# Kernel tuning notes

Hardware: AMD Instinct MI355X
Metric: run time of the kernel (lower is better)

The kernel has to match this reference:

```python
import jax, jax.numpy as jnp
import numpy as np

B, T, N, D = 64, 12, 512, 2      # batch, seq_len, num_nodes, input_dim
R, M, O, H = 64, 64, 1, 12       # rnn_units, message_size, output_dim, horizon


def setup_inputs() -> dict:
    key = jax.random.key(0)
    ks = jax.random.split(key, 12)
    inputs = jax.random.normal(ks[0], (B, T, N, D), jnp.float32)
    h0 = jax.random.normal(ks[1], (N, B, R), jnp.float32)  # torch.randn initial state
    adj = jax.random.uniform(ks[2], (N, N), jnp.float32)
    mask = jax.random.uniform(ks[3], (N, N)) < 0.05
    adj = jnp.where(mask, adj, 0.0)
    s = 1.0 / np.sqrt(R)
    u = lambda k, shape: jax.random.uniform(k, shape, jnp.float32, -s, s)
    return {
        "inputs": inputs, "h0": h0, "adj": adj,
        "W_msg": u(ks[4], (M, R)), "b_msg": u(ks[5], (M,)),
        "W_ih": u(ks[6], (3 * R, D + M)), "W_hh": u(ks[7], (3 * R, R)),
        "b_ih": u(ks[8], (3 * R,)), "b_hh": u(ks[9], (3 * R,)),
        "W_out": u(ks[10], (O * H, R)), "b_out": u(ks[11], (O * H,)),
    }


def reference(inputs, h0, adj, W_msg, b_msg, W_ih, W_hh, b_ih, b_hh, W_out, b_out):
    # mask matches the 'adj[j,i] > 0' guard in the python double loop
    adj_pos = jnp.where(adj > 0.0, adj, 0.0)

    def step(h, x_t):
        # h: [N, B, R]; x_t: [B, N, D]
        hw = h @ W_msg.T + b_msg                       # M_t(h): [N, B, M]
        # m[i] = sum_j adj[j, i] * hw[j]  -> dense masked aggregation
        m = jnp.einsum('ji,jbm->ibm', adj_pos, hw)     # [N, B, M]
        inp2 = jnp.concatenate([m, jnp.transpose(x_t, (1, 0, 2))], axis=2)  # [N, B, M+D]
        # torch GRUCell math (elementwise over the N*B 'batch'):
        gi = inp2 @ W_ih.T + b_ih                      # [N, B, 3R]
        gh = h @ W_hh.T + b_hh                         # [N, B, 3R]
        i_r, i_z, i_n = jnp.split(gi, 3, axis=-1)
        h_r, h_z, h_n = jnp.split(gh, 3, axis=-1)
        r = jax.nn.sigmoid(i_r + h_r)
        z = jax.nn.sigmoid(i_z + h_z)
        n = jnp.tanh(i_n + r * h_n)
        h_new = (1.0 - z) * n + z * h
        return h_new, None

    xs = jnp.transpose(inputs, (1, 0, 2, 3))           # [T, B, N, D]
    h, _ = jax.lax.scan(step, h0, xs)                  # [N, B, R]
    out = h @ W_out.T + b_out                          # R_t(h): [N, B, O*H]
    out = out.reshape(N, B, H, O)                      # reshape(N, B, horizon, -1)
    return jnp.transpose(out, (1, 2, 0, 3))            # [B, H, N, O]
```

## Files before the change

### kernel.cpp

```cpp
#include <hip/hip_runtime.h>

#define Bb 64
#define Tt 12
#define Nn 512
#define Dd 2
#define G3 192
#define Hh 12

typedef float f32x4 __attribute__((ext_vector_type(4)));
typedef _Float16 f16;
typedef _Float16 f16x8 __attribute__((ext_vector_type(8)));

__device__ __forceinline__ int swz4(int row, int bo) {
  return row * 256 + (bo ^ ((row & 7) << 4));
}

__global__ __launch_bounds__(256) void init_kernel(
    const float* __restrict__ adj, const float* __restrict__ W_msg,
    const float* __restrict__ W_ih, const float* __restrict__ W_hh,
    const float* __restrict__ b_ih, const float* __restrict__ b_hh,
    const float* __restrict__ b_msg, f16* __restrict__ g_atf,
    float* __restrict__ g_rowsum, f16* __restrict__ g_w,
    float* __restrict__ g_f) {
  const int bid = blockIdx.x, tid = threadIdx.x, l = tid & 63, wt = tid >> 6;
  if (bid < 32) {
    const int it = bid;
    for (int kt = wt; kt < 16; kt += 4) {
      const int i = (it << 4) + (l & 15);
      const int j0 = (kt << 5) + ((l >> 4) << 3);
      f16* dhi = g_atf + ((it * 16 + kt) * 2 + 0) * 512 + l * 8;
      f16* dlo = g_atf + ((it * 16 + kt) * 2 + 1) * 512 + l * 8;
#pragma unroll
      for (int e = 0; e < 8; ++e) {
        float a = adj[(j0 + e) * Nn + i];
        a = a > 0.f ? a : 0.f;
        const f16 h = (f16)a;
        dhi[e] = h;
        dlo[e] = (f16)(a - (float)h);
      }
    }
    {
      const int i = (it << 4) + (tid >> 4);
      float rs = 0.f;
      for (int j = (tid & 15); j < Nn; j += 16) {
        const float a = adj[j * Nn + i];
        rs += (a > 0.f ? a : 0.f);
      }
      for (int off = 8; off; off >>= 1) rs += __shfl_down(rs, off, 16);
      if ((tid & 15) == 0) g_rowsum[i] = rs;
    }
  } else if (bid == 40) {
    for (int tile = wt; tile < 24; tile += 4) {
      const int nt = tile >> 1, kt = tile & 1;
      const int wrow = nt * 16 + (l & 15);
      const int kc = kt * 32 + ((l >> 4) << 3);
      const float* s2 = W_ih + wrow * 66 + kc;
      const float* s1 = W_hh + wrow * 64 + kc;
#pragma unroll
      for (int j = 0; j < 8; ++j) {
        g_w[tile * 512 + l * 8 + j] = (f16)s2[j];
        g_w[12288 + tile * 512 + l * 8 + j] = (f16)s1[j];
      }
    }
    for (int tile = wt; tile < 8; tile += 4) {
      const int nt = tile >> 1, kt = tile & 1;
      const int wrow = nt * 16 + (l & 15);
      const int kc = kt * 32 + ((l >> 4) << 3);
      const float* s1 = W_msg + wrow * 64 + kc;
#pragma unroll
      for (int j = 0; j < 8; ++j) g_w[24576 + tile * 512 + l * 8 + j] = (f16)s1[j];
    }
    if (tid < G3) {
      g_f[tid * 2] = W_ih[tid * 66 + 64];
      g_f[tid * 2 + 1] = W_ih[tid * 66 + 65];
      g_f[384 + tid] = b_ih[tid];
      g_f[576 + tid] = b_hh[tid];
    }
    if (tid < 64) g_f[768 + tid] = b_msg[tid];
  }
}

__global__ __launch_bounds__(256, 2) void agg_kernel(
    const float* __restrict__ h_src, const f16* __restrict__ g_atf,
    float* __restrict__ s_out) {
  const int bx = blockIdx.x, tid = threadIdx.x, l = tid & 63, wt = tid >> 6;
  const int bi = bx >> 6, bc = bx & 63;
  const int c0 = bc << 6;
  const int it = (bi << 2) + wt;

  const int cl = l & 15;
  const int jk = (l >> 4) << 3;
  const float* hp = h_src + (size_t)jk * 4096 + c0 + cl;
  const f16* ap = g_atf + (it * 16) * 2 * 512 + l * 8;

  f32x4 acc[4];
#pragma unroll
  for (int nt = 0; nt < 4; ++nt) acc[nt] = (f32x4){0.f, 0.f, 0.f, 0.f};

#pragma unroll 4
  for (int kt = 0; kt < 16; ++kt) {
    float v[32];
#pragma unroll
    for (int nt = 0; nt < 4; ++nt)
#pragma unroll
      for (int e = 0; e < 8; ++e)
        v[nt * 8 + e] = hp[(size_t)(kt * 32 + e) * 4096 + nt * 16];

    const f16x8 ahi = *(const f16x8*)(ap + (kt * 2 + 0) * 512);
    const f16x8 alo = *(const f16x8*)(ap + (kt * 2 + 1) * 512);
#pragma unroll
    for (int nt = 0; nt < 4; ++nt) {
      f16x8 bhi, blo;
#pragma unroll
      for (int e = 0; e < 8; ++e) {
        const float x = v[nt * 8 + e];
        const f16 h = (f16)x;
        bhi[e] = h;
        blo[e] = (f16)(x - (float)h);
      }
      acc[nt] = __builtin_amdgcn_mfma_f32_16x16x32_f16(ahi, bhi, acc[nt], 0, 0, 0);
      acc[nt] = __builtin_amdgcn_mfma_f32_16x16x32_f16(alo, bhi, acc[nt], 0, 0, 0);
      acc[nt] = __builtin_amdgcn_mfma_f32_16x16x32_f16(ahi, blo, acc[nt], 0, 0, 0);
    }
  }

  const int ib = (it << 4) + ((l >> 4) << 2);
#pragma unroll
  for (int nt = 0; nt < 4; ++nt) {
    const int col = c0 + (nt << 4) + cl;
#pragma unroll
    for (int g = 0; g < 4; ++g)
      s_out[(ib + g) * 4096 + col] = acc[nt][g];
  }
}

__global__ __launch_bounds__(256, 2) void step_kernel(
    const float* __restrict__ xin, const float* __restrict__ h_src,
    float* __restrict__ h_ws, const float* __restrict__ s_in,
    const uint4* __restrict__ g_blob, const float* __restrict__ g_rowsum,
    const float* __restrict__ W_out, const float* __restrict__ b_out,
    float* __restrict__ out, int t) {
  __shared__ uint4 sBlob[3840];
  __shared__ float m_lds[4096];
  const f16* sBih = (const f16*)sBlob;
  const f16* sBhh = sBih + 12288;
  const f16* sBmsg = sBih + 24576;
  const float* sF = (const float*)(sBih + 28672);
  const float* sWx = sF;
  const float* s_bih = sF + 384;
  const float* s_bhh = sF + 576;
  const float* s_bmsg = sF + 768;

  const int n = blockIdx.x, tid = threadIdx.x, l = tid & 63, wt = tid >> 6;
  const int ar = wt * 16 + (l & 15);
  const int kc = (l >> 4) << 3;

  float x0[4], x1[4];
#pragma unroll
  for (int g = 0; g < 4; ++g) {
    const int brow = wt * 16 + ((l >> 4) << 2) + g;
    const float2 xv = *(const float2*)(xin + ((brow * Tt + t) * Nn + n) * Dd);
    x0[g] = xv.x;
    x1[g] = xv.y;
  }
  const float rsum = g_rowsum[n];
  const float* hrow = h_src + n * 4096;
  const float* srow = s_in + n * 4096;

  f16x8 shi0, slo0, shi1, slo1;
  {
    const float4 q0 = *(const float4*)(srow + ar * 64 + kc);
    const float4 q1 = *(const float4*)(srow + ar * 64 + kc + 4);
    const float4 q2 = *(const float4*)(srow + ar * 64 + 32 + kc);
    const float4 q3 = *(const float4*)(srow + ar * 64 + 36 + kc);
    const float v[16] = {q0.x, q0.y, q0.z, q0.w, q1.x, q1.y, q1.z, q1.w,
                         q2.x, q2.y, q2.z, q2.w, q3.x, q3.y, q3.z, q3.w};
#pragma unroll
    for (int j = 0; j < 8; ++j) {
      f16 h = (f16)v[j];       shi0[j] = h; slo0[j] = (f16)(v[j] - (float)h);
      f16 g = (f16)v[8 + j];   shi1[j] = g; slo1[j] = (f16)(v[8 + j] - (float)g);
    }
  }
  f16x8 ahi0, alo0, ahi1, alo1;
  {
    const float4 q0 = *(const float4*)(hrow + ar * 64 + kc);
    const float4 q1 = *(const float4*)(hrow + ar * 64 + kc + 4);
    const float4 q2 = *(const float4*)(hrow + ar * 64 + 32 + kc);
    const float4 q3 = *(const float4*)(hrow + ar * 64 + 36 + kc);
    const float v[16] = {q0.x, q0.y, q0.z, q0.w, q1.x, q1.y, q1.z, q1.w,
                         q2.x, q2.y, q2.z, q2.w, q3.x, q3.y, q3.z, q3.w};
#pragma unroll
    for (int j = 0; j < 8; ++j) {
      f16 h = (f16)v[j];       ahi0[j] = h; alo0[j] = (f16)(v[j] - (float)h);
      f16 g = (f16)v[8 + j];   ahi1[j] = g; alo1[j] = (f16)(v[8 + j] - (float)g);
    }
  }
  float hreg[4][4];
#pragma unroll
  for (int ct = 0; ct < 4; ++ct)
#pragma unroll
    for (int g = 0; g < 4; ++g) {
      const int row = wt * 16 + ((l >> 4) << 2) + g;
      hreg[ct][g] = hrow[row * 64 + ct * 16 + (l & 15)];
    }
  for (int i = tid; i < 3840; i += 256) sBlob[i] = g_blob[i];
  __syncthreads();

  {
    f32x4 cm[4];
#pragma unroll
    for (int nt = 0; nt < 4; ++nt) {
      cm[nt] = (f32x4){0.f, 0.f, 0.f, 0.f};
      const f16x8 b0 = *(const f16x8*)(sBmsg + (nt * 2 + 0) * 512 + l * 8);
      const f16x8 b1 = *(const f16x8*)(sBmsg + (nt * 2 + 1) * 512 + l * 8);
      cm[nt] = __builtin_amdgcn_mfma_f32_16x16x32_f16(shi0, b0, cm[nt], 0, 0, 0);
      cm[nt] = __builtin_amdgcn_mfma_f32_16x16x32_f16(slo0, b0, cm[nt], 0, 0, 0);
      cm[nt] = __builtin_amdgcn_mfma_f32_16x16x32_f16(shi1, b1, cm[nt], 0, 0, 0);
      cm[nt] = __builtin_amdgcn_mfma_f32_16x16x32_f16(slo1, b1, cm[nt], 0, 0, 0);
    }
#pragma unroll
    for (int nt = 0; nt < 4; ++nt) {
      const int col = nt * 16 + (l & 15);
      const float bm = rsum * s_bmsg[col];
#pragma unroll
      for (int g = 0; g < 4; ++g) {
        const int row = wt * 16 + ((l >> 4) << 2) + g;
        *(float*)((char*)m_lds + swz4(row, col * 4)) = cm[nt][g] + bm;
      }
    }
  }
  f16x8 mhi0, mlo0, mhi1, mlo1;
  {
    const float4 p0 = *(const float4*)((const char*)m_lds + swz4(ar, kc * 4));
    const float4 p1 = *(const float4*)((const char*)m_lds + swz4(ar, kc * 4 + 16));
    const float4 p2 = *(const float4*)((const char*)m_lds + swz4(ar, 128 + kc * 4));
    const float4 p3 = *(const float4*)((const char*)m_lds + swz4(ar, 128 + kc * 4 + 16));
    const float v[16] = {p0.x, p0.y, p0.z, p0.w, p1.x, p1.y, p1.z, p1.w,
                         p2.x, p2.y, p2.z, p2.w, p3.x, p3.y, p3.z, p3.w};
#pragma unroll
    for (int j = 0; j < 8; ++j) {
      f16 h = (f16)v[j];       mhi0[j] = h; mlo0[j] = (f16)(v[j] - (float)h);
      f16 g = (f16)v[8 + j];   mhi1[j] = g; mlo1[j] = (f16)(v[8 + j] - (float)g);
    }
  }

  f32x4 cgi[12], cgh[12];
#pragma unroll
  for (int nt = 0; nt < 12; ++nt) {
    cgi[nt] = (f32x4){0.f, 0.f, 0.f, 0.f};
    cgh[nt] = (f32x4){0.f, 0.f, 0.f, 0.f};
  }
#pragma unroll
  for (int nt = 0; nt < 12; ++nt) {
    const f16x8 bh0 = *(const f16x8*)(sBhh + (nt * 2 + 0) * 512 + l * 8);
    const f16x8 bh1 = *(const f16x8*)(sBhh + (nt * 2 + 1) * 512 + l * 8);
    cgh[nt] = __builtin_amdgcn_mfma_f32_16x16x32_f16(ahi0, bh0, cgh[nt], 0, 0, 0);
    cgh[nt] = __builtin_amdgcn_mfma_f32_16x16x32_f16(alo0, bh0, cgh[nt], 0, 0, 0);
    cgh[nt] = __builtin_amdgcn_mfma_f32_16x16x32_f16(ahi1, bh1, cgh[nt], 0, 0, 0);
    cgh[nt] = __builtin_amdgcn_mfma_f32_16x16x32_f16(alo1, bh1, cgh[nt], 0, 0, 0);
    const f16x8 bi0 = *(const f16x8*)(sBih + (nt * 2 + 0) * 512 + l * 8);
    const f16x8 bi1 = *(const f16x8*)(sBih + (nt * 2 + 1) * 512 + l * 8);
    cgi[nt] = __builtin_amdgcn_mfma_f32_16x16x32_f16(mhi0, bi0, cgi[nt], 0, 0, 0);
    cgi[nt] = __builtin_amdgcn_mfma_f32_16x16x32_f16(mlo0, bi0, cgi[nt], 0, 0, 0);
    cgi[nt] = __builtin_amdgcn_mfma_f32_16x16x32_f16(mhi1, bi1, cgi[nt], 0, 0, 0);
    cgi[nt] = __builtin_amdgcn_mfma_f32_16x16x32_f16(mlo1, bi1, cgi[nt], 0, 0, 0);
  }

#pragma unroll
  for (int ct = 0; ct < 4; ++ct) {
    const int colr = ct * 16 + (l & 15);
    const float wr0 = sWx[colr * 2], wr1 = sWx[colr * 2 + 1];
    const float wz0 = sWx[(colr + 64) * 2], wz1 = sWx[(colr + 64) * 2 + 1];
    const float wn0 = sWx[(colr + 128) * 2], wn1 = sWx[(colr + 128) * 2 + 1];
    const float bir = s_bih[colr], biz = s_bih[colr + 64], bin_ = s_bih[colr + 128];
    const float bhr = s_bhh[colr], bhz = s_bhh[colr + 64], bhn = s_bhh[colr + 128];
#pragma unroll
    for (int g = 0; g < 4; ++g) {
      const int row = wt * 16 + ((l >> 4) << 2) + g;
      const float gir = cgi[ct][g] + x0[g] * wr0 + x1[g] * wr1 + bir;
      const float giz = cgi[ct + 4][g] + x0[g] * wz0 + x1[g] * wz1 + biz;
      const float gin = cgi[ct + 8][g] + x0[g] * wn0 + x1[g] * wn1 + bin_;
      const float ghr = cgh[ct][g] + bhr;
      const float ghz = cgh[ct + 4][g] + bhz;
      const float ghn = cgh[ct + 8][g] + bhn;
      const float rg = 1.f / (1.f + __expf(-(gir + ghr)));
      const float zg = 1.f / (1.f + __expf(-(giz + ghz)));
      const float pa = gin + rg * ghn;
      const float e2 = __expf(-2.f * fabsf(pa));
      float th = (1.f - e2) / (1.f + e2);
      th = copysignf(th, pa);
      const float hn = (1.f - zg) * th + zg * hreg[ct][g];
      if (t < Tt - 1) {
        h_ws[n * 4096 + row * 64 + colr] = hn;
      } else {
        *(float*)((char*)m_lds + swz4(row, colr * 4)) = hn;
      }
    }
  }

  if (t == Tt - 1) {
    f16x8 ohi0, olo0, ohi1, olo1;
    {
      const float4 p0 = *(const float4*)((const char*)m_lds + swz4(ar, kc * 4));
      const float4 p1 = *(const float4*)((const char*)m_lds + swz4(ar, kc * 4 + 16));
      const float4 p2 = *(const float4*)((const char*)m_lds + swz4(ar, 128 + kc * 4));
      const float4 p3 = *(const float4*)((const char*)m_lds + swz4(ar, 128 + kc * 4 + 16));
      const float v[16] = {p0.x, p0.y, p0.z, p0.w, p1.x, p1.y, p1.z, p1.w,
                           p2.x, p2.y, p2.z, p2.w, p3.x, p3.y, p3.z, p3.w};
#pragma unroll
      for (int j = 0; j < 8; ++j) {
        f16 h = (f16)v[j];       ohi0[j] = h; olo0[j] = (f16)(v[j] - (float)h);
        f16 g = (f16)v[8 + j];   ohi1[j] = g; olo1[j] = (f16)(v[8 + j] - (float)g);
      }
    }
    const int o = l & 15;
    f16x8 wo0 = {0, 0, 0, 0, 0, 0, 0, 0}, wo1 = {0, 0, 0, 0, 0, 0, 0, 0};
    if (o < Hh) {
      const float* wr_ = W_out + o * 64 + kc;
      const float4 w0 = *(const float4*)(wr_);
      const float4 w1 = *(const float4*)(wr_ + 4);
      const float4 w2 = *(const float4*)(wr_ + 32);
      const float4 w3 = *(const float4*)(wr_ + 36);
      wo0[0] = (f16)w0.x; wo0[1] = (f16)w0.y; wo0[2] = (f16)w0.z; wo0[3] = (f16)w0.w;
      wo0[4] = (f16)w1.x; wo0[5] = (f16)w1.y; wo0[6] = (f16)w1.z; wo0[7] = (f16)w1.w;
      wo1[0] = (f16)w2.x; wo1[1] = (f16)w2.y; wo1[2] = (f16)w2.z; wo1[3] = (f16)w2.w;
      wo1[4] = (f16)w3.x; wo1[5] = (f16)w3.y; wo1[6] = (f16)w3.z; wo1[7] = (f16)w3.w;
    }
    f32x4 c = {0.f, 0.f, 0.f, 0.f};
    c = __builtin_amdgcn_mfma_f32_16x16x32_f16(ohi0, wo0, c, 0, 0, 0);
    c = __builtin_amdgcn_mfma_f32_16x16x32_f16(olo0, wo0, c, 0, 0, 0);
    c = __builtin_amdgcn_mfma_f32_16x16x32_f16(ohi1, wo1, c, 0, 0, 0);
    c = __builtin_amdgcn_mfma_f32_16x16x32_f16(olo1, wo1, c, 0, 0, 0);
    if (o < Hh) {
      const float bo_ = b_out[o];
#pragma unroll
      for (int g = 0; g < 4; ++g) {
        const int b = wt * 16 + ((l >> 4) << 2) + g;
        out[(b * Hh + o) * Nn + n] = c[g] + bo_;
      }
    }
  }
}

extern "C" void kernel_launch(void* const* d_in, const int* in_sizes, int n_in,
                              void* d_out, int out_size, void* d_ws, size_t ws_size,
                              hipStream_t stream) {
  const float* xin = (const float*)d_in[0];
  const float* h0 = (const float*)d_in[1];
  const float* adj = (const float*)d_in[2];
  const float* W_msg = (const float*)d_in[3];
  const float* b_msg = (const float*)d_in[4];
  const float* W_ih = (const float*)d_in[5];
  const float* W_hh = (const float*)d_in[6];
  const float* b_ih = (const float*)d_in[7];
  const float* b_hh = (const float*)d_in[8];
  const float* W_out = (const float*)d_in[9];
  const float* b_out = (const float*)d_in[10];
  float* out = (float*)d_out;

  char* ws = (char*)d_ws;
  float* h_ws = (float*)ws;
  float* s_buf = (float*)(ws + (8u << 20));
  f16* g_atf = (f16*)(ws + (16u << 20));
  char* base = ws + (17u << 20);
  f16* g_w = (f16*)base;
  float* g_f = (float*)(base + 57344);
  float* g_rowsum = (float*)(base + 61440);
  const uint4* g_blob = (const uint4*)base;

  init_kernel<<<48, 256, 0, stream>>>(adj, W_msg, W_ih, W_hh, b_ih, b_hh,
                                      b_msg, g_atf, g_rowsum, g_w, g_f);
  for (int t = 0; t < Tt; ++t) {
    const float* hs = (t == 0) ? h0 : h_ws;
    agg_kernel<<<512, 256, 0, stream>>>(hs, g_atf, s_buf);
    step_kernel<<<Nn, 256, 0, stream>>>(xin, hs, h_ws, s_buf, g_blob,
                                        g_rowsum, W_out, b_out, out, t);
  }
}
```

Before: 487.3 us.

## Fuse init, aggregation and GRU steps into one persistent kernel with grid barriers

Replaces the init kernel and the 12 pairs of aggregation and step launches with a single persistent kernel of 512 blocks. Phases are separated by a hierarchical atomic grid barrier (16 sub-counters, a root counter and a generation counter). Inside the kernel h0 is copied into the workspace so every timestep reads from one buffer. This removes per-launch overhead and the gaps between 25 dependent kernels. In exchange it depends on all 512 blocks being co-resident, and the barrier has a timeout escape that could silently break synchronisation.

```diff
diff --git a/kernel.cpp b/kernel.cpp
--- a/kernel.cpp
+++ b/kernel.cpp
@@ -6,6 +6,7 @@
 #define Dd 2
 #define G3 192
 #define Hh 12
+#define NSUB 16
 
 typedef float f32x4 __attribute__((ext_vector_type(4)));
 typedef _Float16 f16;
@@ -15,131 +16,45 @@
   return row * 256 + (bo ^ ((row & 7) << 4));
 }
 
-__global__ __launch_bounds__(256) void init_kernel(
+__device__ __forceinline__ void gridbar(int* bar) {
+  __syncthreads();
+  if (threadIdx.x == 0) {
+    int* subs = bar;
+    int* root = bar + NSUB * 32;
+    int* gen = bar + NSUB * 32 + 32;
+    const int g = __hip_atomic_load(gen, __ATOMIC_RELAXED, __HIP_MEMORY_SCOPE_AGENT);
+    const int sub = (int)(blockIdx.x & (NSUB - 1));
+    const int a = __hip_atomic_fetch_add(&subs[sub * 32], 1, __ATOMIC_ACQ_REL,
+                                         __HIP_MEMORY_SCOPE_AGENT);
+    if (a == (Nn / NSUB) - 1) {
+      __hip_atomic_store(&subs[sub * 32], 0, __ATOMIC_RELAXED, __HIP_MEMORY_SCOPE_AGENT);
+      const int r = __hip_atomic_fetch_add(root, 1, __ATOMIC_ACQ_REL,
+                                           __HIP_MEMORY_SCOPE_AGENT);
+      if (r == NSUB - 1) {
+        __hip_atomic_store(root, 0, __ATOMIC_RELAXED, __HIP_MEMORY_SCOPE_AGENT);
+        __hip_atomic_fetch_add(gen, 1, __ATOMIC_RELEASE, __HIP_MEMORY_SCOPE_AGENT);
+      }
+    }
+    const long long t0 = clock64();
+    while (__hip_atomic_load(gen, __ATOMIC_RELAXED, __HIP_MEMORY_SCOPE_AGENT) == g) {
+      __builtin_amdgcn_s_sleep(16);
+      if (clock64() - t0 > 200000000LL) break;
+    }
+    (void)__hip_atomic_load(gen, __ATOMIC_ACQUIRE, __HIP_MEMORY_SCOPE_AGENT);
+  }
+  __syncthreads();
+}
+
+__global__ __launch_bounds__(256, 2) void mpnn_persist(
+    const float* __restrict__ xin, const float* __restrict__ h0,
     const float* __restrict__ adj, const float* __restrict__ W_msg,
     const float* __restrict__ W_ih, const float* __restrict__ W_hh,
     const float* __restrict__ b_ih, const float* __restrict__ b_hh,
-    const float* __restrict__ b_msg, f16* __restrict__ g_atf,
-    float* __restrict__ g_rowsum, f16* __restrict__ g_w,
-    float* __restrict__ g_f) {
-  const int bid = blockIdx.x, tid = threadIdx.x, l = tid & 63, wt = tid >> 6;
-  if (bid < 32) {
-    const int it = bid;
-    for (int kt = wt; kt < 16; kt += 4) {
-      const int i = (it << 4) + (l & 15);
-      const int j0 = (kt << 5) + ((l >> 4) << 3);
-      f16* dhi = g_atf + ((it * 16 + kt) * 2 + 0) * 512 + l * 8;
-      f16* dlo = g_atf + ((it * 16 + kt) * 2 + 1) * 512 + l * 8;
-#pragma unroll
-      for (int e = 0; e < 8; ++e) {
-        float a = adj[(j0 + e) * Nn + i];
-        a = a > 0.f ? a : 0.f;
-        const f16 h = (f16)a;
-        dhi[e] = h;
-        dlo[e] = (f16)(a - (float)h);
-      }
-    }
-    {
-      const int i = (it << 4) + (tid >> 4);
-      float rs = 0.f;
-      for (int j = (tid & 15); j < Nn; j += 16) {
-        const float a = adj[j * Nn + i];
-        rs += (a > 0.f ? a : 0.f);
-      }
-      for (int off = 8; off; off >>= 1) rs += __shfl_down(rs, off, 16);
-      if ((tid & 15) == 0) g_rowsum[i] = rs;
-    }
-  } else if (bid == 40) {
-    for (int tile = wt; tile < 24; tile += 4) {
-      const int nt = tile >> 1, kt = tile & 1;
-      const int wrow = nt * 16 + (l & 15);
-      const int kc = kt * 32 + ((l >> 4) << 3);
-      const float* s2 = W_ih + wrow * 66 + kc;
-      const float* s1 = W_hh + wrow * 64 + kc;
-#pragma unroll
-      for (int j = 0; j < 8; ++j) {
-        g_w[tile * 512 + l * 8 + j] = (f16)s2[j];
-        g_w[12288 + tile * 512 + l * 8 + j] = (f16)s1[j];
-      }
-    }
-    for (int tile = wt; tile < 8; tile += 4) {
-      const int nt = tile >> 1, kt = tile & 1;
-      const int wrow = nt * 16 + (l & 15);
-      const int kc = kt * 32 + ((l >> 4) << 3);
-      const float* s1 = W_msg + wrow * 64 + kc;
-#pragma unroll
-      for (int j = 0; j < 8; ++j) g_w[24576 + tile * 512 + l * 8 + j] = (f16)s1[j];
-    }
-    if (tid < G3) {
-      g_f[tid * 2] = W_ih[tid * 66 + 64];
-      g_f[tid * 2 + 1] = W_ih[tid * 66 + 65];
-      g_f[384 + tid] = b_ih[tid];
-      g_f[576 + tid] = b_hh[tid];
-    }
-    if (tid < 64) g_f[768 + tid] = b_msg[tid];
-  }
-}
-
-__global__ __launch_bounds__(256, 2) void agg_kernel(
-    const float* __restrict__ h_src, const f16* __restrict__ g_atf,
-    float* __restrict__ s_out) {
-  const int bx = blockIdx.x, tid = threadIdx.x, l = tid & 63, wt = tid >> 6;
-  const int bi = bx >> 6, bc = bx & 63;
-  const int c0 = bc << 6;
-  const int it = (bi << 2) + wt;
-
-  const int cl = l & 15;
-  const int jk = (l >> 4) << 3;
-  const float* hp = h_src + (size_t)jk * 4096 + c0 + cl;
-  const f16* ap = g_atf + (it * 16) * 2 * 512 + l * 8;
-
-  f32x4 acc[4];
-#pragma unroll
-  for (int nt = 0; nt < 4; ++nt) acc[nt] = (f32x4){0.f, 0.f, 0.f, 0.f};
-
-#pragma unroll 4
-  for (int kt = 0; kt < 16; ++kt) {
-    float v[32];
-#pragma unroll
-    for (int nt = 0; nt < 4; ++nt)
-#pragma unroll
-      for (int e = 0; e < 8; ++e)
-        v[nt * 8 + e] = hp[(size_t)(kt * 32 + e) * 4096 + nt * 16];
-
-    const f16x8 ahi = *(const f16x8*)(ap + (kt * 2 + 0) * 512);
-    const f16x8 alo = *(const f16x8*)(ap + (kt * 2 + 1) * 512);
-#pragma unroll
-    for (int nt = 0; nt < 4; ++nt) {
-      f16x8 bhi, blo;
-#pragma unroll
-      for (int e = 0; e < 8; ++e) {
-        const float x = v[nt * 8 + e];
-        const f16 h = (f16)x;
-        bhi[e] = h;
-        blo[e] = (f16)(x - (float)h);
-      }
-      acc[nt] = __builtin_amdgcn_mfma_f32_16x16x32_f16(ahi, bhi, acc[nt], 0, 0, 0);
-      acc[nt] = __builtin_amdgcn_mfma_f32_16x16x32_f16(alo, bhi, acc[nt], 0, 0, 0);
-      acc[nt] = __builtin_amdgcn_mfma_f32_16x16x32_f16(ahi, blo, acc[nt], 0, 0, 0);
-    }
-  }
-
-  const int ib = (it << 4) + ((l >> 4) << 2);
-#pragma unroll
-  for (int nt = 0; nt < 4; ++nt) {
-    const int col = c0 + (nt << 4) + cl;
-#pragma unroll
-    for (int g = 0; g < 4; ++g)
-      s_out[(ib + g) * 4096 + col] = acc[nt][g];
-  }
-}
-
-__global__ __launch_bounds__(256, 2) void step_kernel(
-    const float* __restrict__ xin, const float* __restrict__ h_src,
-    float* __restrict__ h_ws, const float* __restrict__ s_in,
-    const uint4* __restrict__ g_blob, const float* __restrict__ g_rowsum,
-    const float* __restrict__ W_out, const float* __restrict__ b_out,
-    float* __restrict__ out, int t) {
+    const float* __restrict__ b_msg, const float* __restrict__ W_out,
+    const float* __restrict__ b_out, float* __restrict__ out,
+    float* __restrict__ h_ws, float* __restrict__ s_buf,
+    f16* __restrict__ g_atf, f16* __restrict__ g_w, float* __restrict__ g_f,
+    float* __restrict__ g_rowsum, int* __restrict__ bar) {
   __shared__ uint4 sBlob[3840];
   __shared__ float m_lds[4096];
   const f16* sBih = (const f16*)sBlob;
@@ -151,192 +66,316 @@
   const float* s_bhh = sF + 576;
   const float* s_bmsg = sF + 768;
 
-  const int n = blockIdx.x, tid = threadIdx.x, l = tid & 63, wt = tid >> 6;
+  const int bx = blockIdx.x, tid = threadIdx.x, l = tid & 63, wt = tid >> 6;
+
+  {
+    const float4* src = (const float4*)(h0 + (size_t)bx * 4096);
+    float4* dst = (float4*)(h_ws + (size_t)bx * 4096);
+    for (int i = tid; i < 1024; i += 256) dst[i] = src[i];
+  }
+  if (bx < 32) {
+    const int it = bx;
+    for (int kt = wt; kt < 16; kt += 4) {
+      const int i = (it << 4) + (l & 15);
+      const int j0 = (kt << 5) + ((l >> 4) << 3);
+      f16* dhi = g_atf + ((it * 16 + kt) * 2 + 0) * 512 + l * 8;
+      f16* dlo = g_atf + ((it * 16 + kt) * 2 + 1) * 512 + l * 8;
+#pragma unroll
+      for (int e = 0; e < 8; ++e) {
+        float a = adj[(j0 + e) * Nn + i];
+        a = a > 0.f ? a : 0.f;
+        const f16 h = (f16)a;
+        dhi[e] = h;
+        dlo[e] = (f16)(a - (float)h);
+      }
+    }
+    {
+      const int i = (it << 4) + (tid >> 4);
+      float rs = 0.f;
+      for (int j = (tid & 15); j < Nn; j += 16) {
+        const float a = adj[j * Nn + i];
+        rs += (a > 0.f ? a : 0.f);
+      }
+      for (int off = 8; off; off >>= 1) rs += __shfl_down(rs, off, 16);
+      if ((tid & 15) == 0) g_rowsum[i] = rs;
+    }
+  } else if (bx == 40) {
+    for (int tile = wt; tile < 24; tile += 4) {
+      const int nt = tile >> 1, kt = tile & 1;
+      const int wrow = nt * 16 + (l & 15);
+      const int kc = kt * 32 + ((l >> 4) << 3);
+      const float* s2 = W_ih + wrow * 66 + kc;
+      const float* s1 = W_hh + wrow * 64 + kc;
+#pragma unroll
+      for (int j = 0; j < 8; ++j) {
+        g_w[tile * 512 + l * 8 + j] = (f16)s2[j];
+        g_w[12288 + tile * 512 + l * 8 + j] = (f16)s1[j];
+      }
+    }
+    for (int tile = wt; tile < 8; tile += 4) {
+      const int nt = tile >> 1, kt = tile & 1;
+      const int wrow = nt * 16 + (l & 15);
+      const int kc = kt * 32 + ((l >> 4) << 3);
+      const float* s1 = W_msg + wrow * 64 + kc;
+#pragma unroll
+      for (int j = 0; j < 8; ++j) g_w[24576 + tile * 512 + l * 8 + j] = (f16)s1[j];
+    }
+    if (tid < G3) {
+      g_f[tid * 2] = W_ih[tid * 66 + 64];
+      g_f[tid * 2 + 1] = W_ih[tid * 66 + 65];
+      g_f[384 + tid] = b_ih[tid];
+      g_f[576 + tid] = b_hh[tid];
+    }
+    if (tid < 64) g_f[768 + tid] = b_msg[tid];
+  }
+  gridbar(bar);
+
+  {
+    const uint4* g_blob = (const uint4*)g_w;
+    for (int i = tid; i < 3840; i += 256) sBlob[i] = g_blob[i];
+  }
+
+  const int n = bx;
   const int ar = wt * 16 + (l & 15);
   const int kc = (l >> 4) << 3;
 
-  float x0[4], x1[4];
-#pragma unroll
-  for (int g = 0; g < 4; ++g) {
-    const int brow = wt * 16 + ((l >> 4) << 2) + g;
-    const float2 xv = *(const float2*)(xin + ((brow * Tt + t) * Nn + n) * Dd);
-    x0[g] = xv.x;
-    x1[g] = xv.y;
-  }
-  const float rsum = g_rowsum[n];
-  const float* hrow = h_src + n * 4096;
-  const float* srow = s_in + n * 4096;
-
-  f16x8 shi0, slo0, shi1, slo1;
-  {
-    const float4 q0 = *(const float4*)(srow + ar * 64 + kc);
-    const float4 q1 = *(const float4*)(srow + ar * 64 + kc + 4);
-    const float4 q2 = *(const float4*)(srow + ar * 64 + 32 + kc);
-    const float4 q3 = *(const float4*)(srow + ar * 64 + 36 + kc);
-    const float v[16] = {q0.x, q0.y, q0.z, q0.w, q1.x, q1.y, q1.z, q1.w,
-                         q2.x, q2.y, q2.z, q2.w, q3.x, q3.y, q3.z, q3.w};
-#pragma unroll
-    for (int j = 0; j < 8; ++j) {
-      f16 h = (f16)v[j];       shi0[j] = h; slo0[j] = (f16)(v[j] - (float)h);
-      f16 g = (f16)v[8 + j];   shi1[j] = g; slo1[j] = (f16)(v[8 + j] - (float)g);
-    }
-  }
-  f16x8 ahi0, alo0, ahi1, alo1;
-  {
-    const float4 q0 = *(const float4*)(hrow + ar * 64 + kc);
-    const float4 q1 = *(const float4*)(hrow + ar * 64 + kc + 4);
-    const float4 q2 = *(const float4*)(hrow + ar * 64 + 32 + kc);
-    const float4 q3 = *(const float4*)(hrow + ar * 64 + 36 + kc);
-    const float v[16] = {q0.x, q0.y, q0.z, q0.w, q1.x, q1.y, q1.z, q1.w,
-                         q2.x, q2.y, q2.z, q2.w, q3.x, q3.y, q3.z, q3.w};
-#pragma unroll
-    for (int j = 0; j < 8; ++j) {
-      f16 h = (f16)v[j];       ahi0[j] = h; alo0[j] = (f16)(v[j] - (float)h);
-      f16 g = (f16)v[8 + j];   ahi1[j] = g; alo1[j] = (f16)(v[8 + j] - (float)g);
-    }
-  }
-  float hreg[4][4];
-#pragma unroll
-  for (int ct = 0; ct < 4; ++ct)
-#pragma unroll
-    for (int g = 0; g < 4; ++g) {
-      const int row = wt * 16 + ((l >> 4) << 2) + g;
-      hreg[ct][g] = hrow[row * 64 + ct * 16 + (l & 15)];
-    }
-  for (int i = tid; i < 3840; i += 256) sBlob[i] = g_blob[i];
-  __syncthreads();
-
-  {
-    f32x4 cm[4];
-#pragma unroll
-    for (int nt = 0; nt < 4; ++nt) {
-      cm[nt] = (f32x4){0.f, 0.f, 0.f, 0.f};
-      const f16x8 b0 = *(const f16x8*)(sBmsg + (nt * 2 + 0) * 512 + l * 8);
-      const f16x8 b1 = *(const f16x8*)(sBmsg + (nt * 2 + 1) * 512 + l * 8);
-      cm[nt] = __builtin_amdgcn_mfma_f32_16x16x32_f16(shi0, b0, cm[nt], 0, 0, 0);
-      cm[nt] = __builtin_amdgcn_mfma_f32_16x16x32_f16(slo0, b0, cm[nt], 0, 0, 0);
-      cm[nt] = __builtin_amdgcn_mfma_f32_16x16x32_f16(shi1, b1, cm[nt], 0, 0, 0);
-      cm[nt] = __builtin_amdgcn_mfma_f32_16x16x32_f16(slo1, b1, cm[nt], 0, 0, 0);
-    }
-#pragma unroll
-    for (int nt = 0; nt < 4; ++nt) {
-      const int col = nt * 16 + (l & 15);
-      const float bm = rsum * s_bmsg[col];
+#pragma unroll 1
+  for (int t = 0; t < Tt; ++t) {
+    {
+      const int bi = bx >> 6, bc = bx & 63;
+      const int c0 = bc << 6;
+      const int it = (bi << 2) + wt;
+      const int cl = l & 15;
+      const int jk = (l >> 4) << 3;
+      const float* hp = h_ws + (size_t)jk * 4096 + c0 + cl;
+      const f16* ap = g_atf + (it * 16) * 2 * 512 + l * 8;
+
+      f32x4 acc[4];
+#pragma unroll
+      for (int nt = 0; nt < 4; ++nt) acc[nt] = (f32x4){0.f, 0.f, 0.f, 0.f};
+
+#pragma unroll 2
+      for (int kt = 0; kt < 16; ++kt) {
+        float v[32];
+#pragma unroll
+        for (int nt = 0; nt < 4; ++nt)
+#pragma unroll
+          for (int e = 0; e < 8; ++e)
+            v[nt * 8 + e] = hp[(size_t)(kt * 32 + e) * 4096 + nt * 16];
+
+        const f16x8 ahi = *(const f16x8*)(ap + (kt * 2 + 0) * 512);
+        const f16x8 alo = *(const f16x8*)(ap + (kt * 2 + 1) * 512);
+#pragma unroll
+        for (int nt = 0; nt < 4; ++nt) {
+          f16x8 bhi, blo;
+#pragma unroll
+          for (int e = 0; e < 8; ++e) {
+            const float x = v[nt * 8 + e];
+            const f16 h = (f16)x;
+            bhi[e] = h;
+            blo[e] = (f16)(x - (float)h);
+          }
+          acc[nt] = __builtin_amdgcn_mfma_f32_16x16x32_f16(ahi, bhi, acc[nt], 0, 0, 0);
+          acc[nt] = __builtin_amdgcn_mfma_f32_16x16x32_f16(alo, bhi, acc[nt], 0, 0, 0);
+          acc[nt] = __builtin_amdgcn_mfma_f32_16x16x32_f16(ahi, blo, acc[nt], 0, 0, 0);
+        }
+      }
+      const int ib = (it << 4) + ((l >> 4) << 2);
+#pragma unroll
+      for (int nt = 0; nt < 4; ++nt) {
+        const int col = c0 + (nt << 4) + cl;
+#pragma unroll
+        for (int g = 0; g < 4; ++g)
+          s_buf[(ib + g) * 4096 + col] = acc[nt][g];
+      }
+    }
+    gridbar(bar);
+
+    {
+      float x0[4], x1[4];
 #pragma unroll
       for (int g = 0; g < 4; ++g) {
-        const int row = wt * 16 + ((l >> 4) << 2) + g;
-        *(float*)((char*)m_lds + swz4(row, col * 4)) = cm[nt][g] + bm;
-      }
-    }
-  }
-  f16x8 mhi0, mlo0, mhi1, mlo1;
-  {
-    const float4 p0 = *(const float4*)((const char*)m_lds + swz4(ar, kc * 4));
-    const float4 p1 = *(const float4*)((const char*)m_lds + swz4(ar, kc * 4 + 16));
-    const float4 p2 = *(const float4*)((const char*)m_lds + swz4(ar, 128 + kc * 4));
-    const float4 p3 = *(const float4*)((const char*)m_lds + swz4(ar, 128 + kc * 4 + 16));
-    const float v[16] = {p0.x, p0.y, p0.z, p0.w, p1.x, p1.y, p1.z, p1.w,
-                         p2.x, p2.y, p2.z, p2.w, p3.x, p3.y, p3.z, p3.w};
-#pragma unroll
-    for (int j = 0; j < 8; ++j) {
-      f16 h = (f16)v[j];       mhi0[j] = h; mlo0[j] = (f16)(v[j] - (float)h);
-      f16 g = (f16)v[8 + j];   mhi1[j] = g; mlo1[j] = (f16)(v[8 + j] - (float)g);
-    }
-  }
-
-  f32x4 cgi[12], cgh[12];
-#pragma unroll
-  for (int nt = 0; nt < 12; ++nt) {
-    cgi[nt] = (f32x4){0.f, 0.f, 0.f, 0.f};
-    cgh[nt] = (f32x4){0.f, 0.f, 0.f, 0.f};
-  }
-#pragma unroll
-  for (int nt = 0; nt < 12; ++nt) {
-    const f16x8 bh0 = *(const f16x8*)(sBhh + (nt * 2 + 0) * 512 + l * 8);
-    const f16x8 bh1 = *(const f16x8*)(sBhh + (nt * 2 + 1) * 512 + l * 8);
-    cgh[nt] = __builtin_amdgcn_mfma_f32_16x16x32_f16(ahi0, bh0, cgh[nt], 0, 0, 0);
-    cgh[nt] = __builtin_amdgcn_mfma_f32_16x16x32_f16(alo0, bh0, cgh[nt], 0, 0, 0);
-    cgh[nt] = __builtin_amdgcn_mfma_f32_16x16x32_f16(ahi1, bh1, cgh[nt], 0, 0, 0);
-    cgh[nt] = __builtin_amdgcn_mfma_f32_16x16x32_f16(alo1, bh1, cgh[nt], 0, 0, 0);
-    const f16x8 bi0 = *(const f16x8*)(sBih + (nt * 2 + 0) * 512 + l * 8);
-    const f16x8 bi1 = *(const f16x8*)(sBih + (nt * 2 + 1) * 512 + l * 8);
-    cgi[nt] = __builtin_amdgcn_mfma_f32_16x16x32_f16(mhi0, bi0, cgi[nt], 0, 0, 0);
-    cgi[nt] = __builtin_amdgcn_mfma_f32_16x16x32_f16(mlo0, bi0, cgi[nt], 0, 0, 0);
-    cgi[nt] = __builtin_amdgcn_mfma_f32_16x16x32_f16(mhi1, bi1, cgi[nt], 0, 0, 0);
-    cgi[nt] = __builtin_amdgcn_mfma_f32_16x16x32_f16(mlo1, bi1, cgi[nt], 0, 0, 0);
-  }
-
-#pragma unroll
-  for (int ct = 0; ct < 4; ++ct) {
-    const int colr = ct * 16 + (l & 15);
-    const float wr0 = sWx[colr * 2], wr1 = sWx[colr * 2 + 1];
-    const float wz0 = sWx[(colr + 64) * 2], wz1 = sWx[(colr + 64) * 2 + 1];
-    const float wn0 = sWx[(colr + 128) * 2], wn1 = sWx[(colr + 128) * 2 + 1];
-    const float bir = s_bih[colr], biz = s_bih[colr + 64], bin_ = s_bih[colr + 128];
-    const float bhr = s_bhh[colr], bhz = s_bhh[colr + 64], bhn = s_bhh[colr + 128];
-#pragma unroll
-    for (int g = 0; g < 4; ++g) {
-      const int row = wt * 16 + ((l >> 4) << 2) + g;
-      const float gir = cgi[ct][g] + x0[g] * wr0 + x1[g] * wr1 + bir;
-      const float giz = cgi[ct + 4][g] + x0[g] * wz0 + x1[g] * wz1 + biz;
-      const float gin = cgi[ct + 8][g] + x0[g] * wn0 + x1[g] * wn1 + bin_;
-      const float ghr = cgh[ct][g] + bhr;
-      const float ghz = cgh[ct + 4][g] + bhz;
-      const float ghn = cgh[ct + 8][g] + bhn;
-      const float rg = 1.f / (1.f + __expf(-(gir + ghr)));
-      const float zg = 1.f / (1.f + __expf(-(giz + ghz)));
-      const float pa = gin + rg * ghn;
-      const float e2 = __expf(-2.f * fabsf(pa));
-      float th = (1.f - e2) / (1.f + e2);
-      th = copysignf(th, pa);
-      const float hn = (1.f - zg) * th + zg * hreg[ct][g];
-      if (t < Tt - 1) {
-        h_ws[n * 4096 + row * 64 + colr] = hn;
+        const int brow = wt * 16 + ((l >> 4) << 2) + g;
+        const float2 xv = *(const float2*)(xin + ((brow * Tt + t) * Nn + n) * Dd);
+        x0[g] = xv.x;
+        x1[g] = xv.y;
+      }
+      const float rsum = g_rowsum[n];
+      const float* hrow = h_ws + (size_t)n * 4096;
+      const float* srow = s_buf + (size_t)n * 4096;
+
+      f16x8 shi0, slo0, shi1, slo1;
+      {
+        const float4 q0 = *(const float4*)(srow + ar * 64 + kc);
+        const float4 q1 = *(const float4*)(srow + ar * 64 + kc + 4);
+        const float4 q2 = *(const float4*)(srow + ar * 64 + 32 + kc);
+        const float4 q3 = *(const float4*)(srow + ar * 64 + 36 + kc);
+        const float v[16] = {q0.x, q0.y, q0.z, q0.w, q1.x, q1.y, q1.z, q1.w,
+                             q2.x, q2.y, q2.z, q2.w, q3.x, q3.y, q3.z, q3.w};
+#pragma unroll
+        for (int j = 0; j < 8; ++j) {
+          f16 h = (f16)v[j];       shi0[j] = h; slo0[j] = (f16)(v[j] - (float)h);
+          f16 g = (f16)v[8 + j];   shi1[j] = g; slo1[j] = (f16)(v[8 + j] - (float)g);
+        }
+      }
+      f16x8 ahi0, alo0, ahi1, alo1;
+      {
+        const float4 q0 = *(const float4*)(hrow + ar * 64 + kc);
+        const float4 q1 = *(const float4*)(hrow + ar * 64 + kc + 4);
+        const float4 q2 = *(const float4*)(hrow + ar * 64 + 32 + kc);
+        const float4 q3 = *(const float4*)(hrow + ar * 64 + 36 + kc);
+        const float v[16] = {q0.x, q0.y, q0.z, q0.w, q1.x, q1.y, q1.z, q1.w,
+                             q2.x, q2.y, q2.z, q2.w, q3.x, q3.y, q3.z, q3.w};
+#pragma unroll
+        for (int j = 0; j < 8; ++j) {
+          f16 h = (f16)v[j];       ahi0[j] = h; alo0[j] = (f16)(v[j] - (float)h);
+          f16 g = (f16)v[8 + j];   ahi1[j] = g; alo1[j] = (f16)(v[8 + j] - (float)g);
+        }
+      }
+      float hreg[4][4];
+#pragma unroll
+      for (int ct = 0; ct < 4; ++ct)
+#pragma unroll
+        for (int g = 0; g < 4; ++g) {
+          const int row = wt * 16 + ((l >> 4) << 2) + g;
+          hreg[ct][g] = hrow[row * 64 + ct * 16 + (l & 15)];
+        }
+
+      {
+        f32x4 cm[4];
+#pragma unroll
+        for (int nt = 0; nt < 4; ++nt) {
+          cm[nt] = (f32x4){0.f, 0.f, 0.f, 0.f};
+          const f16x8 b0 = *(const f16x8*)(sBmsg + (nt * 2 + 0) * 512 + l * 8);
+          const f16x8 b1 = *(const f16x8*)(sBmsg + (nt * 2 + 1) * 512 + l * 8);
+          cm[nt] = __builtin_amdgcn_mfma_f32_16x16x32_f16(shi0, b0, cm[nt], 0, 0, 0);
+          cm[nt] = __builtin_amdgcn_mfma_f32_16x16x32_f16(slo0, b0, cm[nt], 0, 0, 0);
+          cm[nt] = __builtin_amdgcn_mfma_f32_16x16x32_f16(shi1, b1, cm[nt], 0, 0, 0);
+          cm[nt] = __builtin_amdgcn_mfma_f32_16x16x32_f16(slo1, b1, cm[nt], 0, 0, 0);
+        }
+#pragma unroll
+        for (int nt = 0; nt < 4; ++nt) {
+          const int col = nt * 16 + (l & 15);
+          const float bm = rsum * s_bmsg[col];
+#pragma unroll
+          for (int g = 0; g < 4; ++g) {
+            const int row = wt * 16 + ((l >> 4) << 2) + g;
+            *(float*)((char*)m_lds + swz4(row, col * 4)) = cm[nt][g] + bm;
+          }
+        }
+      }
+      f16x8 mhi0, mlo0, mhi1, mlo1;
+      {
+        const float4 p0 = *(const float4*)((const char*)m_lds + swz4(ar, kc * 4));
+        const float4 p1 = *(const float4*)((const char*)m_lds + swz4(ar, kc * 4 + 16));
+        const float4 p2 = *(const float4*)((const char*)m_lds + swz4(ar, 128 + kc * 4));
+        const float4 p3 = *(const float4*)((const char*)m_lds + swz4(ar, 128 + kc * 4 + 16));
+        const float v[16] = {p0.x, p0.y, p0.z, p0.w, p1.x, p1.y, p1.z, p1.w,
+                             p2.x, p2.y, p2.z, p2.w, p3.x, p3.y, p3.z, p3.w};
+#pragma unroll
+        for (int j = 0; j < 8; ++j) {
+          f16 h = (f16)v[j];       mhi0[j] = h; mlo0[j] = (f16)(v[j] - (float)h);
+          f16 g = (f16)v[8 + j];   mlo1[j] = 0; mhi1[j] = g; mlo1[j] = (f16)(v[8 + j] - (float)g);
+        }
+      }
+
+      f32x4 cgi[12], cgh[12];
+#pragma unroll
+      for (int nt = 0; nt < 12; ++nt) {
+        cgi[nt] = (f32x4){0.f, 0.f, 0.f, 0.f};
+        cgh[nt] = (f32x4){0.f, 0.f, 0.f, 0.f};
+      }
+#pragma unroll
+      for (int nt = 0; nt < 12; ++nt) {
+        const f16x8 bh0 = *(const f16x8*)(sBhh + (nt * 2 + 0) * 512 + l * 8);
+        const f16x8 bh1 = *(const f16x8*)(sBhh + (nt * 2 + 1) * 512 + l * 8);
+        cgh[nt] = __builtin_amdgcn_mfma_f32_16x16x32_f16(ahi0, bh0, cgh[nt], 0, 0, 0);
+        cgh[nt] = __builtin_amdgcn_mfma_f32_16x16x32_f16(alo0, bh0, cgh[nt], 0, 0, 0);
+        cgh[nt] = __builtin_amdgcn_mfma_f32_16x16x32_f16(ahi1, bh1, cgh[nt], 0, 0, 0);
+        cgh[nt] = __builtin_amdgcn_mfma_f32_16x16x32_f16(alo1, bh1, cgh[nt], 0, 0, 0);
+        const f16x8 bi0 = *(const f16x8*)(sBih + (nt * 2 + 0) * 512 + l * 8);
+        const f16x8 bi1 = *(const f16x8*)(sBih + (nt * 2 + 1) * 512 + l * 8);
+        cgi[nt] = __builtin_amdgcn_mfma_f32_16x16x32_f16(mhi0, bi0, cgi[nt], 0, 0, 0);
+        cgi[nt] = __builtin_amdgcn_mfma_f32_16x16x32_f16(mlo0, bi0, cgi[nt], 0, 0, 0);
+        cgi[nt] = __builtin_amdgcn_mfma_f32_16x16x32_f16(mhi1, bi1, cgi[nt], 0, 0, 0);
+        cgi[nt] = __builtin_amdgcn_mfma_f32_16x16x32_f16(mlo1, bi1, cgi[nt], 0, 0, 0);
+      }
+
+#pragma unroll
+      for (int ct = 0; ct < 4; ++ct) {
+        const int colr = ct * 16 + (l & 15);
+        const float wr0 = sWx[colr * 2], wr1 = sWx[colr * 2 + 1];
+        const float wz0 = sWx[(colr + 64) * 2], wz1 = sWx[(colr + 64) * 2 + 1];
+        const float wn0 = sWx[(colr + 128) * 2], wn1 = sWx[(colr + 128) * 2 + 1];
+        const float bir = s_bih[colr], biz = s_bih[colr + 64], bin_ = s_bih[colr + 128];
+        const float bhr = s_bhh[colr], bhz = s_bhh[colr + 64], bhn = s_bhh[colr + 128];
+#pragma unroll
+        for (int g = 0; g < 4; ++g) {
+          const int row = wt * 16 + ((l >> 4) << 2) + g;
+          const float gir = cgi[ct][g] + x0[g] * wr0 + x1[g] * wr1 + bir;
+          const float giz = cgi[ct + 4][g] + x0[g] * wz0 + x1[g] * wz1 + biz;
+          const float gin = cgi[ct + 8][g] + x0[g] * wn0 + x1[g] * wn1 + bin_;
+          const float ghr = cgh[ct][g] + bhr;
+          const float ghz = cgh[ct + 4][g] + bhz;
+          const float ghn = cgh[ct + 8][g] + bhn;
+          const float rg = 1.f / (1.f + __expf(-(gir + ghr)));
+          const float zg = 1.f / (1.f + __expf(-(giz + ghz)));
+          const float pa = gin + rg * ghn;
+          const float e2 = __expf(-2.f * fabsf(pa));
+          float th = (1.f - e2) / (1.f + e2);
+          th = copysignf(th, pa);
+          const float hn = (1.f - zg) * th + zg * hreg[ct][g];
+          if (t < Tt - 1) {
+            h_ws[(size_t)n * 4096 + row * 64 + colr] = hn;
+          } else {
+            *(float*)((char*)m_lds + swz4(row, colr * 4)) = hn;
+          }
+        }
+      }
+
+      if (t == Tt - 1) {
+        f16x8 ohi0, olo0, ohi1, olo1;
+        {
+          const float4 p0 = *(const float4*)((const char*)m_lds + swz4(ar, kc * 4));
+          const float4 p1 = *(const float4*)((const char*)m_lds + swz4(ar, kc * 4 + 16));
+          const float4 p2 = *(const float4*)((const char*)m_lds + swz4(ar, 128 + kc * 4));
+          const float4 p3 = *(const float4*)((const char*)m_lds + swz4(ar, 128 + kc * 4 + 16));
+          const float v[16] = {p0.x, p0.y, p0.z, p0.w, p1.x, p1.y, p1.z, p1.w,
+                               p2.x, p2.y, p2.z, p2.w, p3.x, p3.y, p3.z, p3.w};
+#pragma unroll
+          for (int j = 0; j < 8; ++j) {
+            f16 h = (f16)v[j];       ohi0[j] = h; olo0[j] = (f16)(v[j] - (float)h);
+            f16 g = (f16)v[8 + j];   ohi1[j] = g; olo1[j] = (f16)(v[8 + j] - (float)g);
+          }
+        }
+        const int o = l & 15;
+        f16x8 wo0 = {0, 0, 0, 0, 0, 0, 0, 0}, wo1 = {0, 0, 0, 0, 0, 0, 0, 0};
+        if (o < Hh) {
+          const float* wr_ = W_out + o * 64 + kc;
+          const float4 w0 = *(const float4*)(wr_);
+          const float4 w1 = *(const float4*)(wr_ + 4);
+          const float4 w2 = *(const float4*)(wr_ + 32);
+          const float4 w3 = *(const float4*)(wr_ + 36);
+          wo0[0] = (f16)w0.x; wo0[1] = (f16)w0.y; wo0[2] = (f16)w0.z; wo0[3] = (f16)w0.w;
+          wo0[4] = (f16)w1.x; wo0[5] = (f16)w1.y; wo0[6] = (f16)w1.z; wo0[7] = (f16)w1.w;
+          wo1[0] = (f16)w2.x; wo1[1] = (f16)w2.y; wo1[2] = (f16)w2.z; wo1[3] = (f16)w2.w;
+          wo1[4] = (f16)w3.x; wo1[5] = (f16)w3.y; wo1[6] = (f16)w3.z; wo1[7] = (f16)w3.w;
+        }
+        f32x4 c = {0.f, 0.f, 0.f, 0.f};
+        c = __builtin_amdgcn_mfma_f32_16x16x32_f16(ohi0, wo0, c, 0, 0, 0);
+        c = __builtin_amdgcn_mfma_f32_16x16x32_f16(olo0, wo0, c, 0, 0, 0);
+        c = __builtin_amdgcn_mfma_f32_16x16x32_f16(ohi1, wo1, c, 0, 0, 0);
+        c = __builtin_amdgcn_mfma_f32_16x16x32_f16(olo1, wo1, c, 0, 0, 0);
+        if (o < Hh) {
+          const float bo_ = b_out[o];
+#pragma unroll
+          for (int g = 0; g < 4; ++g) {
+            const int b = wt * 16 + ((l >> 4) << 2) + g;
+            out[(b * Hh + o) * Nn + n] = c[g] + bo_;
+          }
+        }
       } else {
-        *(float*)((char*)m_lds + swz4(row, colr * 4)) = hn;
-      }
-    }
-  }
-
-  if (t == Tt - 1) {
-    f16x8 ohi0, olo0, ohi1, olo1;
-    {
-      const float4 p0 = *(const float4*)((const char*)m_lds + swz4(ar, kc * 4));
-      const float4 p1 = *(const float4*)((const char*)m_lds + swz4(ar, kc * 4 + 16));
-      const float4 p2 = *(const float4*)((const char*)m_lds + swz4(ar, 128 + kc * 4));
-      const float4 p3 = *(const float4*)((const char*)m_lds + swz4(ar, 128 + kc * 4 + 16));
-      const float v[16] = {p0.x, p0.y, p0.z, p0.w, p1.x, p1.y, p1.z, p1.w,
-                           p2.x, p2.y, p2.z, p2.w, p3.x, p3.y, p3.z, p3.w};
-#pragma unroll
-      for (int j = 0; j < 8; ++j) {
-        f16 h = (f16)v[j];       ohi0[j] = h; olo0[j] = (f16)(v[j] - (float)h);
-        f16 g = (f16)v[8 + j];   ohi1[j] = g; olo1[j] = (f16)(v[8 + j] - (float)g);
-      }
-    }
-    const int o = l & 15;
-    f16x8 wo0 = {0, 0, 0, 0, 0, 0, 0, 0}, wo1 = {0, 0, 0, 0, 0, 0, 0, 0};
-    if (o < Hh) {
-      const float* wr_ = W_out + o * 64 + kc;
-      const float4 w0 = *(const float4*)(wr_);
-      const float4 w1 = *(const float4*)(wr_ + 4);
-      const float4 w2 = *(const float4*)(wr_ + 32);
-      const float4 w3 = *(const float4*)(wr_ + 36);
-      wo0[0] = (f16)w0.x; wo0[1] = (f16)w0.y; wo0[2] = (f16)w0.z; wo0[3] = (f16)w0.w;
-      wo0[4] = (f16)w1.x; wo0[5] = (f16)w1.y; wo0[6] = (f16)w1.z; wo0[7] = (f16)w1.w;
-      wo1[0] = (f16)w2.x; wo1[1] = (f16)w2.y; wo1[2] = (f16)w2.z; wo1[3] = (f16)w2.w;
-      wo1[4] = (f16)w3.x; wo1[5] = (f16)w3.y; wo1[6] = (f16)w3.z; wo1[7] = (f16)w3.w;
-    }
-    f32x4 c = {0.f, 0.f, 0.f, 0.f};
-    c = __builtin_amdgcn_mfma_f32_16x16x32_f16(ohi0, wo0, c, 0, 0, 0);
-    c = __builtin_amdgcn_mfma_f32_16x16x32_f16(olo0, wo0, c, 0, 0, 0);
-    c = __builtin_amdgcn_mfma_f32_16x16x32_f16(ohi1, wo1, c, 0, 0, 0);
-    c = __builtin_amdgcn_mfma_f32_16x16x32_f16(olo1, wo1, c, 0, 0, 0);
-    if (o < Hh) {
-      const float bo_ = b_out[o];
-#pragma unroll
-      for (int g = 0; g < 4; ++g) {
-        const int b = wt * 16 + ((l >> 4) << 2) + g;
-        out[(b * Hh + o) * Nn + n] = c[g] + bo_;
+        gridbar(bar);
       }
     }
   }
@@ -366,14 +405,10 @@
   f16* g_w = (f16*)base;
   float* g_f = (float*)(base + 57344);
   float* g_rowsum = (float*)(base + 61440);
-  const uint4* g_blob = (const uint4*)base;
-
-  init_kernel<<<48, 256, 0, stream>>>(adj, W_msg, W_ih, W_hh, b_ih, b_hh,
-                                      b_msg, g_atf, g_rowsum, g_w, g_f);
-  for (int t = 0; t < Tt; ++t) {
-    const float* hs = (t == 0) ? h0 : h_ws;
-    agg_kernel<<<512, 256, 0, stream>>>(hs, g_atf, s_buf);
-    step_kernel<<<Nn, 256, 0, stream>>>(xin, hs, h_ws, s_buf, g_blob,
-                                        g_rowsum, W_out, b_out, out, t);
-  }
+  int* bar = (int*)(base + 65536);
+
+  hipMemsetAsync(bar, 0, 4096, stream);
+  mpnn_persist<<<Nn, 256, 0, stream>>>(xin, h0, adj, W_msg, W_ih, W_hh, b_ih,
+                                       b_hh, b_msg, W_out, b_out, out, h_ws,
+                                       s_buf, g_atf, g_w, g_f, g_rowsum, bar);
 }
```

Result: slower. 969.1 us (+98.9%).
